# Kernel optimization log

Hardware: AMD Instinct MI355X
Metric: run time of the kernel (lower is better)

Reference implementation:

```python
import jax, jax.numpy as jnp
import numpy as np

NUM_CLASSES = 80
REG_MAX = 16
CLS_W, BOX_W, DFL_W = 1.0, 2.5, 0.5


def _make_anchors(img=640, strides=(8, 16, 32)):
    pts, strs = [], []
    for s in strides:
        n = img // s
        xs = (np.arange(n, dtype=np.float32) + 0.5) * s
        gy, gx = np.meshgrid(xs, xs, indexing='ij')
        pts.append(np.stack([gx.ravel(), gy.ravel()], axis=1))
        strs.append(np.full((n * n, 1), float(s), np.float32))
    return np.concatenate(pts, 0).astype(np.float32), np.concatenate(strs, 0)


def setup_inputs() -> dict:
    key = jax.random.key(0)
    k1, k2, k3, k4, k5 = jax.random.split(key, 5)
    B, G = 16, 20
    ap, st = _make_anchors()  # A = 8400
    A = ap.shape[0]
    cls_scores = jax.random.uniform(k1, (B, A, NUM_CLASSES), dtype=jnp.float32)
    reg_distri = jax.random.normal(k2, (B, A, 4 * (REG_MAX + 1)), dtype=jnp.float32)
    cxcy = jax.random.uniform(k3, (B, G, 2), dtype=jnp.float32) * 560.0 + 40.0
    wh = jax.random.uniform(k4, (B, G, 2), dtype=jnp.float32) * 120.0 + 20.0
    gt_boxes = jnp.concatenate([cxcy - wh * 0.5, cxcy + wh * 0.5], axis=-1)  # xyxy
    gt_labels = jax.random.randint(k5, (B, G), 0, NUM_CLASSES)
    return {"cls_scores": cls_scores, "reg_distri": reg_distri, "gt_boxes": gt_boxes,
            "anchor_points": jnp.asarray(ap), "stride_tensor": jnp.asarray(st),
            "gt_labels": gt_labels}


def _per_image(pred_cls, pred_reg, gt_boxes, gt_labels, anchor_points, stride):
    A, C = pred_cls.shape
    G = gt_boxes.shape[0]
    k = max(min(13, A // max(G, 1)), 3)
    p = jnp.clip(pred_cls, 1e-7, 1.0 - 1e-7)
    centers = (gt_boxes[:, :2] + gt_boxes[:, 2:]) * 0.5                    # [G,2]
    d = jnp.sqrt(jnp.sum((anchor_points[:, None, :] - centers[None]) ** 2, -1))  # [A,G]
    _, topk_idx = jax.lax.top_k(-d.T, k)                                    # [G,k] nearest anchors
    ax = anchor_points[topk_idx]                                            # [G,k,2]
    inside = ((ax[..., 0] >= gt_boxes[:, None, 0]) & (ax[..., 0] <= gt_boxes[:, None, 2]) &
              (ax[..., 1] >= gt_boxes[:, None, 1]) & (ax[..., 1] <= gt_boxes[:, None, 3]))
    any_in = inside.any(-1, keepdims=True)
    assign_k = jnp.where(any_in, inside, jnp.arange(k) < 3)                 # fallback: 3 nearest
    assign = jnp.zeros((G, A), bool).at[jnp.arange(G)[:, None], topk_idx].set(assign_k)
    aT = assign.T                                                           # [A,G]
    fg = aT.any(1)                                                          # [A]
    last_gt = (G - 1) - jnp.argmax(aT[:, ::-1], axis=1)
    target_box = jnp.where(fg[:, None], gt_boxes[last_gt], 0.0)             # [A,4]
    onehot = jax.nn.one_hot(gt_labels, C, dtype=p.dtype)                    # [G,C]
    target_cls = jnp.max(aT[:, :, None].astype(p.dtype) * onehot[None], axis=1)  # [A,C]
    bce = -(target_cls * jnp.log(p) + (1.0 - target_cls) * jnp.log(1.0 - p))
    num_pos = fg.sum().astype(p.dtype)
    pos_w = jnp.minimum(A / jnp.maximum(num_pos, 1.0), 50.0)
    fgf = fg.astype(p.dtype)[:, None]
    pos_loss = jnp.where(num_pos > 0,
                         jnp.sum(bce * fgf) / jnp.maximum(num_pos * C, 1.0) * pos_w, 0.0)
    neg_loss = jnp.sum(bce * (1.0 - fgf)) / jnp.maximum((A - num_pos) * C, 1.0)
    # box decode (DFL expectation) + smooth-L1 on fg anchors
    reg = jax.nn.softmax(pred_reg.reshape(A, 4, REG_MAX + 1), axis=-1)
    proj = jnp.arange(REG_MAX + 1, dtype=p.dtype)
    dist = jnp.sum(reg * proj, axis=-1)                                     # [A,4]
    s = stride[:, 0]
    pb = jnp.stack([anchor_points[:, 0] - dist[:, 0] * s,
                    anchor_points[:, 1] - dist[:, 1] * s,
                    anchor_points[:, 0] + dist[:, 2] * s,
                    anchor_points[:, 1] + dist[:, 3] * s], axis=-1)
    diff = pb - target_box
    ad = jnp.abs(diff)
    sl1 = jnp.where(ad < 1.0, 0.5 * diff * diff, ad - 0.5)
    box_loss = jnp.where(num_pos > 0,
                         jnp.sum(sl1 * fgf) / jnp.maximum(num_pos * 4.0, 1.0), 0.0)
    return pos_loss + neg_loss, box_loss


def reference(cls_scores, reg_distri, gt_boxes, anchor_points, stride_tensor, gt_labels):
    cls_l, box_l = jax.vmap(
        lambda pc, pr, gb, gl: _per_image(pc, pr, gb, gl, anchor_points, stride_tensor)
    )(cls_scores, reg_distri, gt_boxes, gt_labels)
    loss_cls = cls_l.mean() * CLS_W
    loss_box = box_l.mean() * BOX_W
    return loss_cls + loss_box  # loss_dfl is identically 0 in the original
```

## Files before the change

kernel.cpp:

```cpp
#include <hip/hip_runtime.h>
#include <hip/hip_bf16.h>
#include <cfloat>

#define C_NUM 80
#define CQ 20
#define REG_MAXP1 17
#define NS 33
#define MAXA 8448
#define FG_STRIDE 512
#define FIX_SLOTS (FG_STRIDE * CQ)
#define FG_BLOCKS 48

__device__ inline void cand_for_slot(int sc, float cx, float cy, float& v, int& idx)
{
    v = FLT_MAX; idx = 0x7fffffff;
    int loc, w, n, strd, base;
    if (sc < 36)      { loc = sc;      w = 6; n = 80; strd = 8;  base = 0; }
    else if (sc < 52) { loc = sc - 36; w = 4; n = 40; strd = 16; base = 6400; }
    else if (sc < 68) { loc = sc - 52; w = 4; n = 20; strd = 32; base = 8000; }
    else return;
    float inv = 1.0f / (float)strd;
    int ix0 = (int)floorf(cx * inv - 0.5f) - (w / 2 - 1);
    int iy0 = (int)floorf(cy * inv - 0.5f) - (w / 2 - 1);
    int ix = ix0 + loc % w, iy = iy0 + loc / w;
    if (ix < 0 || ix >= n || iy < 0 || iy >= n) return;
    float ax = ((float)ix + 0.5f) * (float)strd;
    float ay = ((float)iy + 0.5f) * (float)strd;
    float dx = ax - cx, dy = ay - cy;
    v = dx * dx + dy * dy;
    idx = base + iy * n + ix;
}

__global__ __launch_bounds__(1024) void assignraster_kernel(const float* __restrict__ gt_boxes,
                              unsigned int* __restrict__ mask,
                              int* __restrict__ fglist,
                              int* __restrict__ npos,
                              float* __restrict__ acc,
                              unsigned int* __restrict__ counter,
                              int A, int G, int k)
{
    __shared__ unsigned int lmask[8400];
    __shared__ int s_cnt;
    int b = blockIdx.x, t = threadIdx.x;
    int wv = t >> 6, lane = t & 63;

    for (int i = t; i < A; i += 1024) lmask[i] = 0u;
    if (t == 0) s_cnt = 0;
    if (t < 3) acc[b * 3 + t] = 0.f;
    if (b == 0 && t == 0) *counter = 0u;
    __syncthreads();

    for (int g = wv; g < G; g += 16) {
        const float* box = gt_boxes + (size_t)(b * G + g) * 4;
        float x0 = box[0], y0 = box[1], x1 = box[2], y1 = box[3];
        float cx = (x0 + x1) * 0.5f, cy = (y0 + y1) * 0.5f;

        float v0, v1; int i0, i1;
        cand_for_slot(lane,      cx, cy, v0, i0);
        cand_for_slot(lane + 64, cx, cy, v1, i1);

        int my_sel = 0x7fffffff;
        for (int it = 0; it < k; ++it) {
            float lb; int li; bool s0;
            if (v0 < v1 || (v0 == v1 && i0 < i1)) { lb = v0; li = i0; s0 = true; }
            else                                   { lb = v1; li = i1; s0 = false; }
            float rb = lb; int ri = li;
            for (int off = 32; off; off >>= 1) {
                float ov = __shfl_down(rb, off);
                int   oi = __shfl_down(ri, off);
                if (ov < rb || (ov == rb && oi < ri)) { rb = ov; ri = oi; }
            }
            int win = __shfl(ri, 0);
            if (lane == it) my_sel = win;
            if (li == win) {
                if (s0) { v0 = FLT_MAX; i0 = 0x7fffffff; }
                else    { v1 = FLT_MAX; i1 = 0x7fffffff; }
            }
        }

        bool inside = false;
        if (lane < k && my_sel < 0x7fffffff) {
            int idx = my_sel, n, strd, base;
            if (idx < 6400)      { n = 80; strd = 8;  base = 0; }
            else if (idx < 8000) { n = 40; strd = 16; base = 6400; }
            else                 { n = 20; strd = 32; base = 8000; }
            int loc = idx - base;
            float ax = ((float)(loc % n) + 0.5f) * (float)strd;
            float ay = ((float)(loc / n) + 0.5f) * (float)strd;
            inside = (ax >= x0) && (ax <= x1) && (ay >= y0) && (ay <= y1);
        }
        unsigned long long ball = __ballot(inside);
        if (lane < k && my_sel < 0x7fffffff) {
            bool asg = ball ? inside : (lane < 3);
            if (asg) atomicOr(&lmask[my_sel], 1u << g);
        }
    }
    __syncthreads();

    for (int i = t; i < A; i += 1024) {
        unsigned int m = lmask[i];
        mask[(size_t)b * A + i] = m;
        bool fg = (m != 0u);
        unsigned long long bal = __ballot(fg);
        int cnt = __popcll(bal);
        int base = 0;
        if (lane == 0 && cnt) base = atomicAdd(&s_cnt, cnt);
        base = __shfl(base, 0);
        if (fg) {
            int pre = __popcll(bal & ((1ull << lane) - 1ull));
            fglist[b * FG_STRIDE + base + pre] = i | ((31 - __clz(m)) << 16);
        }
    }
    __syncthreads();
    if (t == 0) npos[b] = s_cnt;
}

__global__ __launch_bounds__(256) void assign_kernel(const float* __restrict__ gt_boxes,
                              const float* __restrict__ anchor_points,
                              int* __restrict__ sel,
                              int B, int A, int G, int k)
{
    __shared__ float s_val[4];
    __shared__ int   s_idx[4];
    __shared__ int   s_sel;
    __shared__ int   s_topk[16];
    __shared__ int   s_anyin;

    int bg = blockIdx.x;
    int b = bg / G, g = bg % G;
    const float* box = gt_boxes + (size_t)(b * G + g) * 4;
    float x0 = box[0], y0 = box[1], x1 = box[2], y1 = box[3];
    float cx = (x0 + x1) * 0.5f, cy = (y0 + y1) * 0.5f;

    int t = threadIdx.x;
    float dv[NS];
#pragma unroll
    for (int s = 0; s < NS; ++s) {
        int i = t + s * 256;
        float d = FLT_MAX;
        if (i < A) {
            float dx = anchor_points[2 * i] - cx;
            float dy = anchor_points[2 * i + 1] - cy;
            d = dx * dx + dy * dy;
        }
        dv[s] = d;
    }

    int wid = t >> 6, lane = t & 63;
    for (int it = 0; it < k; ++it) {
        float best = FLT_MAX; int bi = 0x7fffffff;
#pragma unroll
        for (int s = 0; s < NS; ++s) {
            if (dv[s] < best) { best = dv[s]; bi = t + s * 256; }
        }
        for (int off = 32; off; off >>= 1) {
            float ov = __shfl_down(best, off);
            int   oi = __shfl_down(bi, off);
            if (ov < best || (ov == best && oi < bi)) { best = ov; bi = oi; }
        }
        if (lane == 0) { s_val[wid] = best; s_idx[wid] = bi; }
        __syncthreads();
        if (t == 0) {
            float bv = s_val[0]; int bix = s_idx[0];
#pragma unroll
            for (int w = 1; w < 4; ++w) {
                if (s_val[w] < bv || (s_val[w] == bv && s_idx[w] < bix)) { bv = s_val[w]; bix = s_idx[w]; }
            }
            s_sel = bix;
            s_topk[it] = bix;
        }
        __syncthreads();
        int selx = s_sel;
        if ((selx & 255) == t) {
            int slot = selx >> 8;
#pragma unroll
            for (int s = 0; s < NS; ++s) if (s == slot) dv[s] = FLT_MAX;
        }
    }

    if (t == 0) s_anyin = 0;
    __syncthreads();
    bool inside = false; int aidx = -1;
    if (t < k) {
        aidx = s_topk[t];
        float ax = anchor_points[2 * aidx], ay = anchor_points[2 * aidx + 1];
        inside = (ax >= x0) && (ax <= x1) && (ay >= y0) && (ay <= y1);
        if (inside) atomicOr(&s_anyin, 1);
    }
    __syncthreads();
    if (t < k) {
        bool asg = s_anyin ? inside : (t < 3);
        sel[(size_t)bg * 16 + t] = asg ? aidx : -1;
    }
}

__global__ __launch_bounds__(256) void raster_kernel(const int* __restrict__ sel,
                              unsigned int* __restrict__ mask,
                              int* __restrict__ fglist,
                              int* __restrict__ npos,
                              float* __restrict__ acc,
                              unsigned int* __restrict__ counter,
                              int A, int G, int k)
{
    __shared__ unsigned int lmask[MAXA];
    __shared__ int s_cnt;
    int b = blockIdx.x, t = threadIdx.x;

    for (int i = t; i < A; i += 256) lmask[i] = 0u;
    if (t == 0) s_cnt = 0;
    if (t < 3) acc[b * 3 + t] = 0.f;
    if (b == 0 && t == 0) *counter = 0u;
    __syncthreads();

    for (int i = t; i < G * 16; i += 256) {
        int slot = i & 15;
        if (slot < k) {
            int a = sel[(size_t)(b * G) * 16 + i];
            if (a >= 0) atomicOr(&lmask[a], 1u << (i >> 4));
        }
    }
    __syncthreads();

    for (int i = t; i < A; i += 256) {
        unsigned int m = lmask[i];
        mask[(size_t)b * A + i] = m;
        if (m) {
            int lg = 31 - __clz(m);
            int p = atomicAdd(&s_cnt, 1);
            fglist[b * FG_STRIDE + p] = i | (lg << 16);
        }
    }
    __syncthreads();
    if (t == 0) npos[b] = s_cnt;
}

__global__ __launch_bounds__(256) void cls_stream_kernel(const float4* __restrict__ cls,
                           float* __restrict__ acc, int nq)
{
    int b = blockIdx.y;
    const float4* base = cls + (size_t)b * nq;
    int stride = gridDim.x * 256;
    float neg = 0.f;
    for (int q = blockIdx.x * 256 + threadIdx.x; q < nq; q += stride) {
        float4 v = base[q];
        float p0 = fminf(fmaxf(v.x, 1e-7f), 1.0f - 1e-7f);
        float p1 = fminf(fmaxf(v.y, 1e-7f), 1.0f - 1e-7f);
        float p2 = fminf(fmaxf(v.z, 1e-7f), 1.0f - 1e-7f);
        float p3 = fminf(fmaxf(v.w, 1e-7f), 1.0f - 1e-7f);
        neg -= __logf(1.0f - p0) + __logf(1.0f - p1) + __logf(1.0f - p2) + __logf(1.0f - p3);
    }
    for (int off = 32; off; off >>= 1) neg += __shfl_down(neg, off);
    __shared__ float sn[4];
    int wid = threadIdx.x >> 6, lane = threadIdx.x & 63;
    if (lane == 0) sn[wid] = neg;
    __syncthreads();
    if (threadIdx.x == 0) {
        float N = sn[0] + sn[1] + sn[2] + sn[3];
        atomicAdd(&acc[b * 3 + 1], N);
    }
}

__global__ __launch_bounds__(256) void fgfix_kernel(const float4* __restrict__ cls4,
                           const float* __restrict__ reg,
                           const float* __restrict__ gt_boxes,
                           const float* __restrict__ ap,
                           const float* __restrict__ st,
                           const unsigned int* __restrict__ mask,
                           const int* __restrict__ gt_labels,
                           const int* __restrict__ fglist,
                           const int* __restrict__ npos,
                           float* __restrict__ acc,
                           unsigned int* __restrict__ counter,
                           float* __restrict__ out,
                           int A, int G, int B)
{
    int b = blockIdx.y;
    int idx = blockIdx.x * 256 + threadIdx.x;
    int np = npos[b];
    float posAdd = 0.f, negSub = 0.f, bx = 0.f;

    if (idx < FIX_SLOTS) {
        int e = idx / CQ, cq = idx - e * CQ;
        if (e < np) {
            int ent = fglist[b * FG_STRIDE + e];
            int a = ent & 0xffff;
            unsigned int m = mask[(size_t)b * A + a];
            const int* lab = gt_labels + (size_t)b * G;
            int c0 = cq * 4;
            float4 v = cls4[(size_t)b * A * CQ + (size_t)a * CQ + cq];
            float p0 = fminf(fmaxf(v.x, 1e-7f), 1.0f - 1e-7f);
            float p1 = fminf(fmaxf(v.y, 1e-7f), 1.0f - 1e-7f);
            float p2 = fminf(fmaxf(v.z, 1e-7f), 1.0f - 1e-7f);
            float p3 = fminf(fmaxf(v.w, 1e-7f), 1.0f - 1e-7f);
            unsigned int tm = 0, mm = m;
            while (mm) {
                int g = __ffs(mm) - 1;
                mm &= mm - 1;
                unsigned int d = (unsigned int)(lab[g] - c0);
                if (d < 4u) tm |= 1u << d;
            }
            float n0 = -__logf(1.0f - p0), n1 = -__logf(1.0f - p1);
            float n2 = -__logf(1.0f - p2), n3 = -__logf(1.0f - p3);
            negSub = n0 + n1 + n2 + n3;
            posAdd  = (tm & 1u) ? -__logf(p0) : n0;
            posAdd += (tm & 2u) ? -__logf(p1) : n1;
            posAdd += (tm & 4u) ? -__logf(p2) : n2;
            posAdd += (tm & 8u) ? -__logf(p3) : n3;
        }
    } else {
        int idx2 = idx - FIX_SLOTS;
        int e = idx2 >> 2, j = idx2 & 3;
        if (e < np) {
            int ent = fglist[b * FG_STRIDE + e];
            int a = ent & 0xffff;
            int lg = ent >> 16;
            float tbj = gt_boxes[(size_t)(b * G + lg) * 4 + j];
            const float* rj = reg + ((size_t)b * A + a) * (4 * REG_MAXP1) + j * REG_MAXP1;
            float rr[REG_MAXP1];
#pragma unroll
            for (int i = 0; i < REG_MAXP1; ++i) rr[i] = rj[i];
            float mx = rr[0];
#pragma unroll
            for (int i = 1; i < REG_MAXP1; ++i) mx = fmaxf(mx, rr[i]);
            float sum = 0.f, dot = 0.f;
#pragma unroll
            for (int i = 0; i < REG_MAXP1; ++i) {
                float ev = __expf(rr[i] - mx);
                sum += ev; dot += ev * (float)i;
            }
            float dist = dot / sum;
            float s = st[a];
            float ac = ap[2 * a + (j & 1)];
            float pbj = (j < 2) ? (ac - dist * s) : (ac + dist * s);
            float df = pbj - tbj;
            float ad = fabsf(df);
            bx = (ad < 1.0f) ? 0.5f * df * df : ad - 0.5f;
        }
    }

    for (int off = 32; off; off >>= 1) {
        posAdd += __shfl_down(posAdd, off);
        negSub += __shfl_down(negSub, off);
        bx     += __shfl_down(bx, off);
    }
    __shared__ float sp[4], sn[4], sb[4];
    __shared__ int s_last;
    int wid = threadIdx.x >> 6, lane = threadIdx.x & 63;
    if (lane == 0) { sp[wid] = posAdd; sn[wid] = negSub; sb[wid] = bx; }
    __syncthreads();
    if (threadIdx.x == 0) {
        float P = sp[0] + sp[1] + sp[2] + sp[3];
        float N = sn[0] + sn[1] + sn[2] + sn[3];
        float X = sb[0] + sb[1] + sb[2] + sb[3];
        if (P != 0.f) atomicAdd(&acc[b * 3 + 0], P);
        if (N != 0.f) atomicAdd(&acc[b * 3 + 1], -N);
        if (X != 0.f) atomicAdd(&acc[b * 3 + 2], X);
        __threadfence();
        unsigned int old = atomicAdd(counter, 1u);
        s_last = (old == (unsigned int)(gridDim.x * gridDim.y) - 1u) ? 1 : 0;
    }
    __syncthreads();

    if (s_last) {
        int t = threadIdx.x;
        float cls_c = 0.f, box_c = 0.f;
        if (t < 64) {
            for (int bb = t; bb < B; bb += 64) {
                float a0 = atomicAdd(&acc[bb * 3 + 0], 0.f);
                float a1 = atomicAdd(&acc[bb * 3 + 1], 0.f);
                float a2 = atomicAdd(&acc[bb * 3 + 2], 0.f);
                float npf = (float)npos[bb];
                float neg = a1 / fmaxf(((float)A - npf) * (float)C_NUM, 1.0f);
                float pos = 0.f, box = 0.f;
                if (npf > 0.f) {
                    float pw = fminf((float)A / fmaxf(npf, 1.0f), 50.0f);
                    pos = a0 / fmaxf(npf * (float)C_NUM, 1.0f) * pw;
                    box = a2 / fmaxf(npf * 4.0f, 1.0f);
                }
                cls_c += pos + neg;
                box_c += box;
            }
            for (int off = 32; off; off >>= 1) {
                cls_c += __shfl_down(cls_c, off);
                box_c += __shfl_down(box_c, off);
            }
            if (t == 0) out[0] = cls_c / (float)B * 1.0f + box_c / (float)B * 2.5f;
        }
    }
}

extern "C" void kernel_launch(void* const* d_in, const int* in_sizes, int n_in,
                              void* d_out, int out_size, void* d_ws, size_t ws_size,
                              hipStream_t stream)
{
    const float* cls   = (const float*)d_in[0];
    const float* reg   = (const float*)d_in[1];
    const float* gtb   = (const float*)d_in[2];
    const float* ap    = (const float*)d_in[3];
    const float* st    = (const float*)d_in[4];
    const int*   glab  = (const int*)d_in[5];

    int A = in_sizes[3] / 2;
    int B = in_sizes[0] / (A * C_NUM);
    int G = in_sizes[5] / B;
    int k = A / (G > 1 ? G : 1); if (k > 13) k = 13; if (k < 3) k = 3;

    unsigned int* mask = (unsigned int*)d_ws;
    float* acc   = (float*)(mask + (size_t)B * A);
    int*   npos  = (int*)(acc + 3 * B);
    int*   sel   = npos + B;
    int*   fgl   = sel + (size_t)B * G * 16;
    unsigned int* counter = (unsigned int*)(fgl + (size_t)B * FG_STRIDE);

    if (A == 8400 && G <= 32) {
        assignraster_kernel<<<B, 1024, 0, stream>>>(gtb, mask, fgl, npos, acc, counter, A, G, k);
    } else {
        assign_kernel<<<B * G, 256, 0, stream>>>(gtb, ap, sel, B, A, G, k);
        raster_kernel<<<B, 256, 0, stream>>>(sel, mask, fgl, npos, acc, counter, A, G, k);
    }

    dim3 g3(128, B);
    cls_stream_kernel<<<g3, 256, 0, stream>>>((const float4*)cls, acc, A * CQ);

    dim3 g4(FG_BLOCKS, B);
    fgfix_kernel<<<g4, 256, 0, stream>>>((const float4*)cls, reg, gtb, ap, st,
                                         mask, glab, fgl, npos, acc, counter,
                                         (float*)d_out, A, G, B);
}
```

Baseline: 153.6 us.

## Fuse foreground fixups into assignment kernel and merge final reduction into cls stream

The per-image assignment kernel now keeps the foreground list and mask in shared memory and computes the positive-class and box losses for foreground anchors directly, so the global mask and fglist are no longer written. The dense negative-log streaming kernel now also does the last-block final reduction, which drops the separate fgfix kernel launch on the fast path. Launches go from three to two, at the cost of doing the foreground work in only B blocks instead of spreading it across a wider grid.

```diff
diff --git a/kernel.cpp b/kernel.cpp
--- a/kernel.cpp
+++ b/kernel.cpp
@@ -31,22 +31,26 @@
     idx = base + iy * n + ix;
 }
 
-__global__ __launch_bounds__(1024) void assignraster_kernel(const float* __restrict__ gt_boxes,
-                              unsigned int* __restrict__ mask,
-                              int* __restrict__ fglist,
+__global__ __launch_bounds__(1024) void assignfix_kernel(const float* __restrict__ gt_boxes,
+                              const float4* __restrict__ cls4,
+                              const float* __restrict__ reg,
+                              const float* __restrict__ ap,
+                              const float* __restrict__ st,
+                              const int* __restrict__ gt_labels,
                               int* __restrict__ npos,
                               float* __restrict__ acc,
                               unsigned int* __restrict__ counter,
                               int A, int G, int k)
 {
     __shared__ unsigned int lmask[8400];
+    __shared__ int s_ent[FG_STRIDE];
     __shared__ int s_cnt;
+    __shared__ float sp[16], sn[16], sb[16];
     int b = blockIdx.x, t = threadIdx.x;
     int wv = t >> 6, lane = t & 63;
 
     for (int i = t; i < A; i += 1024) lmask[i] = 0u;
     if (t == 0) s_cnt = 0;
-    if (t < 3) acc[b * 3 + t] = 0.f;
     if (b == 0 && t == 0) *counter = 0u;
     __syncthreads();
 
@@ -99,7 +103,6 @@
 
     for (int i = t; i < A; i += 1024) {
         unsigned int m = lmask[i];
-        mask[(size_t)b * A + i] = m;
         bool fg = (m != 0u);
         unsigned long long bal = __ballot(fg);
         int cnt = __popcll(bal);
@@ -108,11 +111,147 @@
         base = __shfl(base, 0);
         if (fg) {
             int pre = __popcll(bal & ((1ull << lane) - 1ull));
-            fglist[b * FG_STRIDE + base + pre] = i | ((31 - __clz(m)) << 16);
-        }
-    }
-    __syncthreads();
-    if (t == 0) npos[b] = s_cnt;
+            s_ent[base + pre] = i | ((31 - __clz(m)) << 16);
+        }
+    }
+    __syncthreads();
+    int np = s_cnt;
+    if (t == 0) npos[b] = np;
+
+    const int* lab = gt_labels + (size_t)b * G;
+    float posAdd = 0.f, negSub = 0.f, bx = 0.f;
+    for (int i = t; i < np * CQ; i += 1024) {
+        int e = i / CQ, cq = i - e * CQ;
+        int ent = s_ent[e];
+        int a = ent & 0xffff;
+        unsigned int m = lmask[a];
+        int c0 = cq * 4;
+        float4 v = cls4[(size_t)b * A * CQ + (size_t)a * CQ + cq];
+        float p0 = fminf(fmaxf(v.x, 1e-7f), 1.0f - 1e-7f);
+        float p1 = fminf(fmaxf(v.y, 1e-7f), 1.0f - 1e-7f);
+        float p2 = fminf(fmaxf(v.z, 1e-7f), 1.0f - 1e-7f);
+        float p3 = fminf(fmaxf(v.w, 1e-7f), 1.0f - 1e-7f);
+        unsigned int tm = 0, mm = m;
+        while (mm) {
+            int g = __ffs(mm) - 1;
+            mm &= mm - 1;
+            unsigned int d = (unsigned int)(lab[g] - c0);
+            if (d < 4u) tm |= 1u << d;
+        }
+        float n0 = -__logf(1.0f - p0), n1 = -__logf(1.0f - p1);
+        float n2 = -__logf(1.0f - p2), n3 = -__logf(1.0f - p3);
+        negSub += n0 + n1 + n2 + n3;
+        posAdd += (tm & 1u) ? -__logf(p0) : n0;
+        posAdd += (tm & 2u) ? -__logf(p1) : n1;
+        posAdd += (tm & 4u) ? -__logf(p2) : n2;
+        posAdd += (tm & 8u) ? -__logf(p3) : n3;
+    }
+
+    for (int i = t; i < np * 4; i += 1024) {
+        int e = i >> 2, j = i & 3;
+        int ent = s_ent[e];
+        int a = ent & 0xffff;
+        int lg = ent >> 16;
+        float tbj = gt_boxes[(size_t)(b * G + lg) * 4 + j];
+        const float* rj = reg + ((size_t)b * A + a) * (4 * REG_MAXP1) + j * REG_MAXP1;
+        float rr[REG_MAXP1];
+#pragma unroll
+        for (int ii = 0; ii < REG_MAXP1; ++ii) rr[ii] = rj[ii];
+        float mx = rr[0];
+#pragma unroll
+        for (int ii = 1; ii < REG_MAXP1; ++ii) mx = fmaxf(mx, rr[ii]);
+        float sum = 0.f, dot = 0.f;
+#pragma unroll
+        for (int ii = 0; ii < REG_MAXP1; ++ii) {
+            float ev = __expf(rr[ii] - mx);
+            sum += ev; dot += ev * (float)ii;
+        }
+        float dist = dot / sum;
+        float s = st[a];
+        float ac = ap[2 * a + (j & 1)];
+        float pbj = (j < 2) ? (ac - dist * s) : (ac + dist * s);
+        float df = pbj - tbj;
+        float ad = fabsf(df);
+        bx += (ad < 1.0f) ? 0.5f * df * df : ad - 0.5f;
+    }
+
+    for (int off = 32; off; off >>= 1) {
+        posAdd += __shfl_down(posAdd, off);
+        negSub += __shfl_down(negSub, off);
+        bx     += __shfl_down(bx, off);
+    }
+    if (lane == 0) { sp[wv] = posAdd; sn[wv] = negSub; sb[wv] = bx; }
+    __syncthreads();
+    if (t == 0) {
+        float P = 0.f, N = 0.f, X = 0.f;
+#pragma unroll
+        for (int w = 0; w < 16; ++w) { P += sp[w]; N += sn[w]; X += sb[w]; }
+        acc[b * 3 + 0] = P;
+        acc[b * 3 + 1] = -N;
+        acc[b * 3 + 2] = X;
+    }
+}
+
+__global__ __launch_bounds__(256) void cls_final_kernel(const float4* __restrict__ cls,
+                           const int* __restrict__ npos,
+                           float* __restrict__ acc,
+                           unsigned int* __restrict__ counter,
+                           float* __restrict__ out,
+                           int nq, int A, int B)
+{
+    int b = blockIdx.y;
+    const float4* base = cls + (size_t)b * nq;
+    int stride = gridDim.x * 256;
+    float neg = 0.f;
+    for (int q = blockIdx.x * 256 + threadIdx.x; q < nq; q += stride) {
+        float4 v = base[q];
+        float p0 = fminf(fmaxf(v.x, 1e-7f), 1.0f - 1e-7f);
+        float p1 = fminf(fmaxf(v.y, 1e-7f), 1.0f - 1e-7f);
+        float p2 = fminf(fmaxf(v.z, 1e-7f), 1.0f - 1e-7f);
+        float p3 = fminf(fmaxf(v.w, 1e-7f), 1.0f - 1e-7f);
+        neg -= __logf(1.0f - p0) + __logf(1.0f - p1) + __logf(1.0f - p2) + __logf(1.0f - p3);
+    }
+    for (int off = 32; off; off >>= 1) neg += __shfl_down(neg, off);
+    __shared__ float sn[4];
+    __shared__ int s_last;
+    int wid = threadIdx.x >> 6, lane = threadIdx.x & 63;
+    if (lane == 0) sn[wid] = neg;
+    __syncthreads();
+    if (threadIdx.x == 0) {
+        float N = sn[0] + sn[1] + sn[2] + sn[3];
+        atomicAdd(&acc[b * 3 + 1], N);
+        __threadfence();
+        unsigned int old = atomicAdd(counter, 1u);
+        s_last = (old == (unsigned int)(gridDim.x * gridDim.y) - 1u) ? 1 : 0;
+    }
+    __syncthreads();
+
+    if (s_last) {
+        int t = threadIdx.x;
+        float cls_c = 0.f, box_c = 0.f;
+        if (t < 64) {
+            for (int bb = t; bb < B; bb += 64) {
+                float a0 = atomicAdd(&acc[bb * 3 + 0], 0.f);
+                float a1 = atomicAdd(&acc[bb * 3 + 1], 0.f);
+                float a2 = atomicAdd(&acc[bb * 3 + 2], 0.f);
+                float npf = (float)npos[bb];
+                float negL = a1 / fmaxf(((float)A - npf) * (float)C_NUM, 1.0f);
+                float pos = 0.f, box = 0.f;
+                if (npf > 0.f) {
+                    float pw = fminf((float)A / fmaxf(npf, 1.0f), 50.0f);
+                    pos = a0 / fmaxf(npf * (float)C_NUM, 1.0f) * pw;
+                    box = a2 / fmaxf(npf * 4.0f, 1.0f);
+                }
+                cls_c += pos + negL;
+                box_c += box;
+            }
+            for (int off = 32; off; off >>= 1) {
+                cls_c += __shfl_down(cls_c, off);
+                box_c += __shfl_down(box_c, off);
+            }
+            if (t == 0) out[0] = cls_c / (float)B * 1.0f + box_c / (float)B * 2.5f;
+        }
+    }
 }
 
 __global__ __launch_bounds__(256) void assign_kernel(const float* __restrict__ gt_boxes,
@@ -370,14 +509,14 @@
                 float a1 = atomicAdd(&acc[bb * 3 + 1], 0.f);
                 float a2 = atomicAdd(&acc[bb * 3 + 2], 0.f);
                 float npf = (float)npos[bb];
-                float neg = a1 / fmaxf(((float)A - npf) * (float)C_NUM, 1.0f);
+                float negL = a1 / fmaxf(((float)A - npf) * (float)C_NUM, 1.0f);
                 float pos = 0.f, box = 0.f;
                 if (npf > 0.f) {
                     float pw = fminf((float)A / fmaxf(npf, 1.0f), 50.0f);
                     pos = a0 / fmaxf(npf * (float)C_NUM, 1.0f) * pw;
                     box = a2 / fmaxf(npf * 4.0f, 1.0f);
                 }
-                cls_c += pos + neg;
+                cls_c += pos + negL;
                 box_c += box;
             }
             for (int off = 32; off; off >>= 1) {
@@ -413,17 +552,19 @@
     unsigned int* counter = (unsigned int*)(fgl + (size_t)B * FG_STRIDE);
 
     if (A == 8400 && G <= 32) {
-        assignraster_kernel<<<B, 1024, 0, stream>>>(gtb, mask, fgl, npos, acc, counter, A, G, k);
+        assignfix_kernel<<<B, 1024, 0, stream>>>(gtb, (const float4*)cls, reg, ap, st,
+                                                 glab, npos, acc, counter, A, G, k);
+        dim3 g2(128, B);
+        cls_final_kernel<<<g2, 256, 0, stream>>>((const float4*)cls, npos, acc, counter,
+                                                 (float*)d_out, A * CQ, A, B);
     } else {
         assign_kernel<<<B * G, 256, 0, stream>>>(gtb, ap, sel, B, A, G, k);
         raster_kernel<<<B, 256, 0, stream>>>(sel, mask, fgl, npos, acc, counter, A, G, k);
-    }
-
-    dim3 g3(128, B);
-    cls_stream_kernel<<<g3, 256, 0, stream>>>((const float4*)cls, acc, A * CQ);
-
-    dim3 g4(FG_BLOCKS, B);
-    fgfix_kernel<<<g4, 256, 0, stream>>>((const float4*)cls, reg, gtb, ap, st,
-                                         mask, glab, fgl, npos, acc, counter,
-                                         (float*)d_out, A, G, B);
-}
+        dim3 g3(128, B);
+        cls_stream_kernel<<<g3, 256, 0, stream>>>((const float4*)cls, acc, A * CQ);
+        dim3 g4(FG_BLOCKS, B);
+        fgfix_kernel<<<g4, 256, 0, stream>>>((const float4*)cls, reg, gtb, ap, st,
+                                             mask, glab, fgl, npos, acc, counter,
+                                             (float*)d_out, A, G, B);
+    }
+}
```

Result: slower. 187.7 us (+22.2%).
